# Kernel optimization log

Hardware: AMD Instinct MI355X
Metric: run time of the kernel (lower is better)

The kernel has to match this reference:

```python
import math
import jax, jax.numpy as jnp
import numpy as np

B, N, C = 2, 2048, 1024
H = 16
D = C // H  # 64
LN_EPS = 1e-5


def setup_inputs() -> dict:
    key = jax.random.key(0)
    ks = jax.random.split(key, 5)
    x = jax.random.normal(ks[0], (B, N, C), dtype=jnp.float32)
    w_qkv = jax.random.normal(ks[1], (C, 3 * C), dtype=jnp.float32) * 0.02
    w_proj = jax.random.normal(ks[2], (C, C), dtype=jnp.float32) * 0.02
    b_proj = jnp.zeros((C,), dtype=jnp.float32)
    ln_w = jnp.ones((D,), dtype=jnp.float32) + jax.random.normal(ks[3], (D,), dtype=jnp.float32) * 0.02
    ln_b = jax.random.normal(ks[4], (D,), dtype=jnp.float32) * 0.02
    return {"x": x, "w_qkv": w_qkv, "w_proj": w_proj, "b_proj": b_proj,
            "ln_w": ln_w, "ln_b": ln_b}


def _layernorm(t, w, b):
    mu = jnp.mean(t, axis=-1, keepdims=True)
    var = jnp.var(t, axis=-1, keepdims=True)
    return (t - mu) * jax.lax.rsqrt(var + LN_EPS) * w + b


def reference(x, w_qkv, w_proj, b_proj, ln_w, ln_b):
    b, n, c = x.shape
    h, d = H, c // H
    # QKV projection (no bias): [b,n,3c] -> [3,b,h,n,d]
    qkv = (x @ w_qkv).reshape(b, n, 3, h, d).transpose(2, 0, 3, 1, 4)
    q, k, v = qkv[0], qkv[1], qkv[2]
    # per-head LayerNorm on q and k (qk_norm)
    q = _layernorm(q, ln_w, ln_b)
    k = _layernorm(k, ln_w, ln_b)
    # NOTE: source multiplies q by sqrt(head_dim) (faithful to original)
    q = q * jnp.asarray(math.sqrt(d), dtype=q.dtype)
    scores = jnp.einsum('bhnd,bhmd->bhnm', q, k)  # [b,h,n,n]
    mask_value = -jnp.finfo(scores.dtype).max
    causal = jnp.tril(jnp.ones((n, n), dtype=bool))
    scores = jnp.where(causal, scores, mask_value)
    attn = jax.nn.softmax(scores, axis=-1)
    out = jnp.einsum('bhnm,bhmd->bhnd', attn, v)  # [b,h,n,d]
    out = out.transpose(0, 2, 1, 3).reshape(b, n, c)  # b n (h d)
    return out @ w_proj + b_proj
```

## Files before the change

### kernel.cpp

```cpp
#include <hip/hip_runtime.h>

#define LOG2E 1.4426950408889634f

typedef _Float16 f16x8_t __attribute__((ext_vector_type(8)));
typedef _Float16 f16x4_t __attribute__((ext_vector_type(4)));
typedef float    f32x4_t __attribute__((ext_vector_type(4)));

#define MFMA32(a, b, c) __builtin_amdgcn_mfma_f32_16x16x32_f16(a, b, c, 0, 0, 0)
#define MFMA16(a, b, c) __builtin_amdgcn_mfma_f32_16x16x16f16(a, b, c, 0, 0, 0)

__device__ __forceinline__ void async_copy16(void* lds, const void* g) {
    __builtin_amdgcn_global_load_lds(
        (const __attribute__((address_space(1))) unsigned char*)g,
        (__attribute__((address_space(3))) unsigned char*)lds, 16, 0, 0);
}

__global__ void cast_f32_f16_k(const float* __restrict__ in, _Float16* __restrict__ out, int n4) {
    int i = blockIdx.x * blockDim.x + threadIdx.x;
    if (i >= n4) return;
    float4 v = ((const float4*)in)[i];
    f16x4_t o = { (_Float16)v.x, (_Float16)v.y, (_Float16)v.z, (_Float16)v.w };
    ((f16x4_t*)out)[i] = o;
}

__global__ void transpose_cast_k(const float* __restrict__ in, _Float16* __restrict__ out,
                                 int R, int C) {
    __shared__ _Float16 tl[64][65];
    const int t = threadIdx.x;
    const int c = t & 63;
    const int r4 = t >> 6;
    const int r0 = blockIdx.y * 64, c0 = blockIdx.x * 64;
#pragma unroll
    for (int i = 0; i < 16; ++i) {
        int r = r4 + i * 4;
        tl[c][r] = (_Float16)in[(size_t)(r0 + r) * C + c0 + c];
    }
    __syncthreads();
#pragma unroll
    for (int i = 0; i < 16; ++i) {
        int rr = r4 + i * 4;
        out[(size_t)(c0 + rr) * R + r0 + c] = tl[rr][c];
    }
}

__global__ void vtrans_k(const _Float16* __restrict__ qkv, _Float16* __restrict__ VTg) {
    __shared__ _Float16 tl[64][65];
    const int t = threadIdx.x;
    const int bh = blockIdx.x;
    const int b = bh >> 4, h = bh & 15;
    const int n0 = blockIdx.y * 64;
    const int c = t & 63;
    const int r4 = t >> 6;
#pragma unroll
    for (int i = 0; i < 16; ++i) {
        int r = r4 + i * 4;
        tl[c][r] = qkv[(size_t)(b * 2048 + n0 + r) * 3072 + 2048 + h * 64 + c];
    }
    __syncthreads();
#pragma unroll
    for (int i = 0; i < 16; ++i) {
        int d = r4 + i * 4;
        VTg[(size_t)bh * 131072 + (size_t)d * 2048 + n0 + c] = tl[d][c];
    }
}

template <typename OutT, bool BIAS>
__global__ __launch_bounds__(256, 2)
void gemm_f16_k(const _Float16* __restrict__ A, const _Float16* __restrict__ BT,
                OutT* __restrict__ C, const float* __restrict__ bias,
                int M, int N, int K) {
    __shared__ _Float16 As[2][128][32];
    __shared__ _Float16 Bs[2][128][32];
    const int tid = threadIdx.x;
    const int wid = tid >> 6, lane = tid & 63;
    const int qd = lane >> 4, ln = lane & 15;
    const int m0 = blockIdx.x * 128, n0 = blockIdx.y * 128;
    const int wm = (wid >> 1) * 64, wn = (wid & 1) * 64;

    f32x4_t acc[4][4] = {};

    const int srow = lane >> 2;
    const int skk  = (lane & 3) * 8;

    for (int k0 = 0; k0 < K; k0 += 64) {
        __syncthreads();
#pragma unroll
        for (int p = 0; p < 4; ++p) {
            const int seg = p * 4 + wid;
            const int s   = seg >> 3;
            const int rg  = seg & 7;
            const int row = rg * 16 + srow;
            const size_t goff = (size_t)row * K + k0 + s * 32 + skk;
            async_copy16(&As[0][0][0] + seg * 512, A  + (size_t)m0 * K + goff);
            async_copy16(&Bs[0][0][0] + seg * 512, BT + (size_t)n0 * K + goff);
        }
        __syncthreads();
#pragma unroll
        for (int s = 0; s < 2; ++s) {
            f16x8_t a[4], b[4];
#pragma unroll
            for (int i = 0; i < 4; ++i)
                a[i] = *(const f16x8_t*)&As[s][wm + i * 16 + ln][qd * 8];
#pragma unroll
            for (int j = 0; j < 4; ++j)
                b[j] = *(const f16x8_t*)&Bs[s][wn + j * 16 + ln][qd * 8];
#pragma unroll
            for (int i = 0; i < 4; ++i)
#pragma unroll
                for (int j = 0; j < 4; ++j)
                    acc[i][j] = MFMA32(a[i], b[j], acc[i][j]);
        }
    }
#pragma unroll
    for (int i = 0; i < 4; ++i)
#pragma unroll
        for (int j = 0; j < 4; ++j) {
            const int col = n0 + wn + j * 16 + ln;
            const float bv = BIAS ? bias[col] : 0.0f;
#pragma unroll
            for (int r = 0; r < 4; ++r) {
                const int row = m0 + wm + i * 16 + qd * 4 + r;
                C[(size_t)row * N + col] = (OutT)(acc[i][j][r] + bv);
            }
        }
}

__global__ __launch_bounds__(256, 2)
void gemm_f16_m64_k(const _Float16* __restrict__ A, const _Float16* __restrict__ BT,
                    float* __restrict__ C, const float* __restrict__ bias,
                    int M, int N, int K) {
    __shared__ _Float16 As[2][64][32];
    __shared__ _Float16 Bs[2][128][32];
    const int tid = threadIdx.x;
    const int wid = tid >> 6, lane = tid & 63;
    const int qd = lane >> 4, ln = lane & 15;
    const int m0 = blockIdx.x * 64, n0 = blockIdx.y * 128;
    const int wn = wid * 32;

    f32x4_t acc[4][2] = {};
    const int srow = lane >> 2;
    const int skk  = (lane & 3) * 8;

    for (int k0 = 0; k0 < K; k0 += 64) {
        __syncthreads();
#pragma unroll
        for (int p = 0; p < 2; ++p) {
            const int seg = p * 4 + wid;
            const int hidx = seg * 512 + lane * 8;
            const int s_ = hidx >> 11;
            const int row = (hidx >> 5) & 63;
            const int kk = hidx & 31;
            async_copy16(&As[0][0][0] + seg * 512,
                         A + (size_t)(m0 + row) * K + k0 + s_ * 32 + kk);
        }
#pragma unroll
        for (int p = 0; p < 4; ++p) {
            const int seg = p * 4 + wid;
            const int s   = seg >> 3;
            const int rg  = seg & 7;
            const int row = rg * 16 + srow;
            async_copy16(&Bs[0][0][0] + seg * 512,
                         BT + (size_t)(n0 + row) * K + k0 + s * 32 + skk);
        }
        __syncthreads();
#pragma unroll
        for (int s = 0; s < 2; ++s) {
            f16x8_t a[4], b[2];
#pragma unroll
            for (int i = 0; i < 4; ++i)
                a[i] = *(const f16x8_t*)&As[s][i * 16 + ln][qd * 8];
#pragma unroll
            for (int j = 0; j < 2; ++j)
                b[j] = *(const f16x8_t*)&Bs[s][wn + j * 16 + ln][qd * 8];
#pragma unroll
            for (int i = 0; i < 4; ++i)
#pragma unroll
                for (int j = 0; j < 2; ++j)
                    acc[i][j] = MFMA32(a[i], b[j], acc[i][j]);
        }
    }
#pragma unroll
    for (int i = 0; i < 4; ++i)
#pragma unroll
        for (int j = 0; j < 2; ++j) {
            const int col = n0 + wn + j * 16 + ln;
            const float bv = bias[col];
#pragma unroll
            for (int r = 0; r < 4; ++r) {
                const int row = m0 + i * 16 + qd * 4 + r;
                C[(size_t)row * N + col] = acc[i][j][r] + bv;
            }
        }
}

__global__ void ln_qk_k(const _Float16* __restrict__ qkv, const float* __restrict__ ln_w,
                        const float* __restrict__ ln_b, _Float16* __restrict__ Qb,
                        _Float16* __restrict__ Kb) {
    const int tid = threadIdx.x;
    const int wid = tid >> 6, lane = tid & 63;
    const int row = blockIdx.x * 4 + wid;
    const int t = row >> 4;
    const int h = row & 15;
    const int b = t >> 11, n = t & 2047;
    const size_t base = (size_t)t * 3072 + h * 64 + lane;
    float q = (float)qkv[base];
    float k = (float)qkv[base + 1024];
    const float wv = ln_w[lane], bv = ln_b[lane];

    float sq = q, sk = k;
#pragma unroll
    for (int m = 1; m < 64; m <<= 1) { sq += __shfl_xor(sq, m); sk += __shfl_xor(sk, m); }
    sq *= (1.0f / 64.0f); sk *= (1.0f / 64.0f);
    const float dq = q - sq, dk = k - sk;
    float vq = dq * dq, vk = dk * dk;
#pragma unroll
    for (int m = 1; m < 64; m <<= 1) { vq += __shfl_xor(vq, m); vk += __shfl_xor(vk, m); }
    vq *= (1.0f / 64.0f); vk *= (1.0f / 64.0f);
    const float yq = dq * rsqrtf(vq + 1e-5f) * wv + bv;
    const float yk = dk * rsqrtf(vk + 1e-5f) * wv + bv;
    const size_t obase = ((size_t)((b * 16 + h) * 2048 + n)) * 64 + lane;
    Qb[obase] = (_Float16)(yq * (8.0f * LOG2E));
    Kb[obase] = (_Float16)yk;
}

__global__ __launch_bounds__(256, 3)
void attn_part_k(const _Float16* __restrict__ Q, const _Float16* __restrict__ K,
                 const _Float16* __restrict__ VTg, _Float16* __restrict__ O,
                 float* __restrict__ Op, float* __restrict__ ml) {
    __shared__ _Float16 Ks[2][2][64][32];
    __shared__ _Float16 VT[2][64][64];

    const int tid = threadIdx.x;
    const int wid = tid >> 6, lane = tid & 63;
    const int qd = lane >> 4, ln = lane & 15;
    const int bh = blockIdx.x;
    const int b = bh >> 4, h = bh & 15;
    const int y = blockIdx.y;
    int band, chunk, nst;
    if (y < 16)      { band = 16 + y; chunk = 0; nst = 16; }
    else if (y < 32) { band = 47 - y; chunk = 1; nst = band - 15; }
    else             { band = 47 - y; chunk = 0; nst = band + 1; }
    const size_t kvbase = (size_t)bh * 2048 * 64;
    const size_t vtbase = (size_t)bh * 131072;
    const int qrow0 = band * 64 + wid * 16;
    const int kvbeg = chunk * 1024;

    f16x8_t qf[2];
#pragma unroll
    for (int s = 0; s < 2; ++s)
        qf[s] = *(const f16x8_t*)&Q[kvbase + (size_t)(qrow0 + ln) * 64 + s * 32 + qd * 8];

    f32x4_t o[4] = {};
    float m = -3.0e38f, l = 0.0f;

    const int vrow = lane >> 3;
    const int vY   = (lane & 7) ^ (vrow & 7);
    const int khidx_base = lane * 8;

    auto stage = [&](int buf, int kv0) {
#pragma unroll
        for (int p = 0; p < 2; ++p) {
            const int seg = p * 4 + wid;
            const int hidx = seg * 512 + khidx_base;
            const int s_ = hidx >> 11;
            const int rrow = (hidx >> 5) & 63;
            const int kk = hidx & 31;
            async_copy16(&Ks[buf][0][0][0] + seg * 512,
                         K + kvbase + (size_t)(kv0 + rrow) * 64 + s_ * 32 + kk);
        }
#pragma unroll
        for (int p = 0; p < 2; ++p) {
            const int seg = p * 4 + wid;
            const int d = seg * 8 + vrow;
            async_copy16(&VT[buf][0][0] + seg * 512,
                         VTg + vtbase + (size_t)d * 2048 + kv0 + vY * 8);
        }
    };

    stage(0, kvbeg);

    for (int st = 0; st < nst; ++st) {
        const int kv0 = kvbeg + st * 64;
        __syncthreads();
        if (st + 1 < nst) stage((st + 1) & 1, kv0 + 64);
        const int buf = st & 1;

        f16x8_t kb[4][2];
#pragma unroll
        for (int jt = 0; jt < 4; ++jt)
#pragma unroll
            for (int s = 0; s < 2; ++s)
                kb[jt][s] = *(const f16x8_t*)&Ks[buf][s][jt * 16 + ln][qd * 8];
        f16x4_t vf[4][4];
#pragma unroll
        for (int dt = 0; dt < 4; ++dt)
#pragma unroll
            for (int c = 0; c < 4; ++c)
                vf[dt][c] = *(const f16x4_t*)
                    &VT[buf][dt * 16 + ln][(((2 * c + (qd >> 1)) ^ (ln & 7)) << 3) + (qd & 1) * 4];

        f32x4_t sc[4];
#pragma unroll
        for (int jt = 0; jt < 4; ++jt) {
            f32x4_t s = {};
            s = MFMA32(kb[jt][0], qf[0], s);
            s = MFMA32(kb[jt][1], qf[1], s);
            sc[jt] = s;
        }
        if (chunk * 16 + st == band) {
            const int qq = qrow0 + ln;
#pragma unroll
            for (int c = 0; c < 4; ++c)
#pragma unroll
                for (int r = 0; r < 4; ++r)
                    if (kv0 + c * 16 + qd * 4 + r > qq) sc[c][r] = -3.0e38f;
        }
        float mx = sc[0][0];
#pragma unroll
        for (int c = 0; c < 4; ++c)
#pragma unroll
            for (int r = 0; r < 4; ++r) mx = fmaxf(mx, sc[c][r]);
        mx = fmaxf(mx, __shfl_xor(mx, 16));
        mx = fmaxf(mx, __shfl_xor(mx, 32));
        const float mn = fmaxf(m, mx);
        const float al = exp2f(m - mn);
        m = mn;
        float rs = 0.0f;
        f16x4_t pf[4];
#pragma unroll
        for (int c = 0; c < 4; ++c)
#pragma unroll
            for (int r = 0; r < 4; ++r) {
                const float p = exp2f(sc[c][r] - mn);
                rs += p;
                pf[c][r] = (_Float16)p;
            }
        l = l * al + rs;
#pragma unroll
        for (int dt = 0; dt < 4; ++dt) o[dt] *= al;
#pragma unroll
        for (int dt = 0; dt < 4; ++dt)
#pragma unroll
            for (int c = 0; c < 4; ++c)
                o[dt] = MFMA16(vf[dt][c], pf[c], o[dt]);
    }

    float lt = l + __shfl_xor(l, 16);
    lt = lt + __shfl_xor(lt, 32);

    if (band < 16) {
        const float inv = 1.0f / lt;
        const size_t base = ((size_t)(b * 2048 + qrow0 + ln)) * 1024 + h * 64 + qd * 4;
#pragma unroll
        for (int dt = 0; dt < 4; ++dt) {
            f16x4_t ov;
#pragma unroll
            for (int r = 0; r < 4; ++r) ov[r] = (_Float16)(o[dt][r] * inv);
            *(f16x4_t*)&O[base + dt * 16] = ov;
        }
    } else {
        const size_t pb = (((size_t)bh * 16 + (band - 16)) * 2 + chunk);
        const int row = wid * 16 + ln;
        float* op = Op + pb * 4096 + (size_t)row * 64 + qd * 4;
#pragma unroll
        for (int dt = 0; dt < 4; ++dt)
            *(f32x4_t*)&op[dt * 16] = o[dt];
        if (qd == 0) {
            ml[pb * 128 + row * 2]     = m;
            ml[pb * 128 + row * 2 + 1] = lt;
        }
    }
}

__global__ __launch_bounds__(256)
void attn_merge_k(const float* __restrict__ Op, const float* __restrict__ ml,
                  _Float16* __restrict__ O) {
    const int bh = blockIdx.x, bnd = blockIdx.y;
    const int b = bh >> 4, h = bh & 15;
    const int band = 16 + bnd;
    const size_t pb = ((size_t)bh * 16 + bnd) * 2;
    const int tid = threadIdx.x;
    const int row = tid >> 2;
    const int c4 = (tid & 3) * 16;
    const float m0 = ml[pb * 128 + row * 2],     l0 = ml[pb * 128 + row * 2 + 1];
    const float m1 = ml[pb * 128 + 128 + row * 2], l1 = ml[pb * 128 + 128 + row * 2 + 1];
    const float mm = fmaxf(m0, m1);
    const float a0 = exp2f(m0 - mm), a1 = exp2f(m1 - mm);
    const float inv = 1.0f / (l0 * a0 + l1 * a1);
    const float* p0 = Op + pb * 4096 + (size_t)row * 64 + c4;
    const float* p1 = p0 + 4096;
    _Float16* op = O + ((size_t)(b * 2048 + band * 64 + row)) * 1024 + h * 64 + c4;
#pragma unroll
    for (int g = 0; g < 4; ++g) {
        f32x4_t v0 = *(const f32x4_t*)&p0[g * 4];
        f32x4_t v1 = *(const f32x4_t*)&p1[g * 4];
        f16x4_t ov;
#pragma unroll
        for (int r = 0; r < 4; ++r)
            ov[r] = (_Float16)((v0[r] * a0 + v1[r] * a1) * inv);
        *(f16x4_t*)&op[g * 4] = ov;
    }
}

extern "C" void kernel_launch(void* const* d_in, const int* in_sizes, int n_in,
                              void* d_out, int out_size, void* d_ws, size_t ws_size,
                              hipStream_t stream) {
    const float* x      = (const float*)d_in[0];
    const float* w_qkv  = (const float*)d_in[1];
    const float* w_proj = (const float*)d_in[2];
    const float* b_proj = (const float*)d_in[3];
    const float* ln_w   = (const float*)d_in[4];
    const float* ln_b   = (const float*)d_in[5];
    float* out = (float*)d_out;

    char* w = (char*)d_ws;
    _Float16*  qkv    = (_Float16*)w;  w += (size_t)4096 * 3072 * 2;
    _Float16*  xh     = (_Float16*)w;  w += (size_t)4096 * 1024 * 2;
    _Float16*  wqkvT  = (_Float16*)w;  w += (size_t)3072 * 1024 * 2;
    _Float16*  wprojT = (_Float16*)w;  w += (size_t)1024 * 1024 * 2;
    _Float16*  Qb     = (_Float16*)w;  w += (size_t)32 * 2048 * 64 * 2;
    _Float16*  Kb     = (_Float16*)w;  w += (size_t)32 * 2048 * 64 * 2;
    _Float16*  VTg    = (_Float16*)w;  w += (size_t)32 * 64 * 2048 * 2;
    _Float16*  Ah     = (_Float16*)w;  w += (size_t)4096 * 1024 * 2;
    float*     Op     = (float*)w;     w += (size_t)32 * 16 * 2 * 4096 * 4;
    float*     mlb    = (float*)w;     w += (size_t)32 * 16 * 2 * 128 * 4;

    cast_f32_f16_k<<<4096, 256, 0, stream>>>(x, xh, 4096 * 1024 / 4);
    transpose_cast_k<<<dim3(48, 16), 256, 0, stream>>>(w_qkv, wqkvT, 1024, 3072);
    transpose_cast_k<<<dim3(16, 16), 256, 0, stream>>>(w_proj, wprojT, 1024, 1024);
    gemm_f16_k<_Float16, false><<<dim3(32, 24), 256, 0, stream>>>(xh, wqkvT, qkv, nullptr, 4096, 3072, 1024);
    vtrans_k<<<dim3(32, 32), 256, 0, stream>>>(qkv, VTg);
    ln_qk_k<<<16384, 256, 0, stream>>>(qkv, ln_w, ln_b, Qb, Kb);
    attn_part_k<<<dim3(32, 48), 256, 0, stream>>>(Qb, Kb, VTg, Ah, Op, mlb);
    attn_merge_k<<<dim3(32, 16), 256, 0, stream>>>(Op, mlb, Ah);
    gemm_f16_m64_k<<<dim3(64, 8), 256, 0, stream>>>(Ah, wprojT, out, b_proj, 4096, 1024, 1024);
}
```

Before: 210.0 us.

## Widen attention query tile to 128 rows and pre-swizzle V tiles in global

The attention kernel now has each wave handle 32 query rows (two 16-row fragments), so every staged K/V tile is reused across twice as many queries. The causal work split is rebalanced into 128-row bands, with long bands split across two KV chunks and later merged. vtrans_k now writes V^T in tile-contiguous, pre-swizzled order, so staging becomes a linear copy and LDS reads use 8-wide vectors. Softmax probabilities are packed with cvt_pkrtz. In exchange, register pressure grows and the grid has fewer blocks, which may lower occupancy and worsen load balance.

```diff
diff --git a/kernel.cpp b/kernel.cpp
--- a/kernel.cpp
+++ b/kernel.cpp
@@ -4,6 +4,7 @@
 
 typedef _Float16 f16x8_t __attribute__((ext_vector_type(8)));
 typedef _Float16 f16x4_t __attribute__((ext_vector_type(4)));
+typedef _Float16 f16x2_t __attribute__((ext_vector_type(2)));
 typedef float    f32x4_t __attribute__((ext_vector_type(4)));
 
 #define MFMA32(a, b, c) __builtin_amdgcn_mfma_f32_16x16x32_f16(a, b, c, 0, 0, 0)
@@ -44,23 +45,30 @@
 }
 
 __global__ void vtrans_k(const _Float16* __restrict__ qkv, _Float16* __restrict__ VTg) {
-    __shared__ _Float16 tl[64][65];
-    const int t = threadIdx.x;
+    __shared__ _Float16 tl[64][68];
+    const int tid = threadIdx.x;
     const int bh = blockIdx.x;
     const int b = bh >> 4, h = bh & 15;
-    const int n0 = blockIdx.y * 64;
-    const int c = t & 63;
-    const int r4 = t >> 6;
+    const int t = blockIdx.y;
+    const int c = tid & 63;
+    const int r4 = tid >> 6;
 #pragma unroll
     for (int i = 0; i < 16; ++i) {
         int r = r4 + i * 4;
-        tl[c][r] = qkv[(size_t)(b * 2048 + n0 + r) * 3072 + 2048 + h * 64 + c];
+        tl[c][r] = qkv[(size_t)(b * 2048 + t * 64 + r) * 3072 + 2048 + h * 64 + c];
     }
     __syncthreads();
-#pragma unroll
-    for (int i = 0; i < 16; ++i) {
-        int d = r4 + i * 4;
-        VTg[(size_t)bh * 131072 + (size_t)d * 2048 + n0 + c] = tl[d][c];
+    const size_t obase = (size_t)bh * 131072 + (size_t)t * 4096;
+#pragma unroll
+    for (int e = 0; e < 2; ++e) {
+        const int ci = tid * 2 + e;
+        const int d = ci >> 3, w = ci & 7;
+        const int pq = w ^ (d & 7);
+        const int base = (pq >> 2) * 32 + (pq & 3) * 4;
+        f16x4_t v0 = *(const f16x4_t*)&tl[d][base];
+        f16x4_t v1 = *(const f16x4_t*)&tl[d][base + 16];
+        f16x8_t val = __builtin_shufflevector(v0, v1, 0, 1, 2, 3, 4, 5, 6, 7);
+        *(f16x8_t*)&VTg[obase + ci * 8] = val;
     }
 }
 
@@ -236,32 +244,28 @@
     const int bh = blockIdx.x;
     const int b = bh >> 4, h = bh & 15;
     const int y = blockIdx.y;
-    int band, chunk, nst;
-    if (y < 16)      { band = 16 + y; chunk = 0; nst = 16; }
-    else if (y < 32) { band = 47 - y; chunk = 1; nst = band - 15; }
-    else             { band = 47 - y; chunk = 0; nst = band + 1; }
+    int band, chunk, nst, kvbeg;
+    if (y < 16) { band = 15 - (y >> 1); chunk = y & 1; nst = band + 1; kvbeg = chunk * nst * 64; }
+    else        { band = 7 - (y - 16);  chunk = -1;    nst = 2 * (band + 1); kvbeg = 0; }
     const size_t kvbase = (size_t)bh * 2048 * 64;
     const size_t vtbase = (size_t)bh * 131072;
-    const int qrow0 = band * 64 + wid * 16;
-    const int kvbeg = chunk * 1024;
-
-    f16x8_t qf[2];
-#pragma unroll
-    for (int s = 0; s < 2; ++s)
-        qf[s] = *(const f16x8_t*)&Q[kvbase + (size_t)(qrow0 + ln) * 64 + s * 32 + qd * 8];
-
-    f32x4_t o[4] = {};
-    float m = -3.0e38f, l = 0.0f;
-
-    const int vrow = lane >> 3;
-    const int vY   = (lane & 7) ^ (vrow & 7);
-    const int khidx_base = lane * 8;
+    const int qrow0 = band * 128 + wid * 32;
+
+    f16x8_t qf[2][2];
+#pragma unroll
+    for (int f = 0; f < 2; ++f)
+#pragma unroll
+        for (int s = 0; s < 2; ++s)
+            qf[f][s] = *(const f16x8_t*)&Q[kvbase + (size_t)(qrow0 + f * 16 + ln) * 64 + s * 32 + qd * 8];
+
+    f32x4_t o[2][4] = {};
+    float m[2] = { -3.0e38f, -3.0e38f }, l[2] = { 0.0f, 0.0f };
 
     auto stage = [&](int buf, int kv0) {
 #pragma unroll
         for (int p = 0; p < 2; ++p) {
-            const int seg = p * 4 + wid;
-            const int hidx = seg * 512 + khidx_base;
+            const int seg = wid * 2 + p;
+            const int hidx = seg * 512 + lane * 8;
             const int s_ = hidx >> 11;
             const int rrow = (hidx >> 5) & 63;
             const int kk = hidx & 31;
@@ -270,10 +274,9 @@
         }
 #pragma unroll
         for (int p = 0; p < 2; ++p) {
-            const int seg = p * 4 + wid;
-            const int d = seg * 8 + vrow;
+            const int seg = wid * 2 + p;
             async_copy16(&VT[buf][0][0] + seg * 512,
-                         VTg + vtbase + (size_t)d * 2048 + kv0 + vY * 8);
+                         VTg + vtbase + (size_t)kv0 * 64 + seg * 512 + lane * 8);
         }
     };
 
@@ -291,83 +294,97 @@
 #pragma unroll
             for (int s = 0; s < 2; ++s)
                 kb[jt][s] = *(const f16x8_t*)&Ks[buf][s][jt * 16 + ln][qd * 8];
-        f16x4_t vf[4][4];
+        f16x8_t vf8[4][2];
 #pragma unroll
         for (int dt = 0; dt < 4; ++dt)
 #pragma unroll
+            for (int pp = 0; pp < 2; ++pp) {
+                const int w = (pp * 4 + qd) ^ (ln & 7);
+                vf8[dt][pp] = *(const f16x8_t*)&VT[buf][dt * 16 + ln][w * 8];
+            }
+
+#pragma unroll
+        for (int f = 0; f < 2; ++f) {
+            f32x4_t sc[4];
+#pragma unroll
+            for (int jt = 0; jt < 4; ++jt) {
+                f32x4_t s = {};
+                s = MFMA32(kb[jt][0], qf[f][0], s);
+                s = MFMA32(kb[jt][1], qf[f][1], s);
+                sc[jt] = s;
+            }
+            const int qbase = qrow0 + f * 16;
+            if (kv0 + 63 > qbase) {
+                const int qq = qbase + ln;
+#pragma unroll
+                for (int c = 0; c < 4; ++c)
+#pragma unroll
+                    for (int r = 0; r < 4; ++r)
+                        if (kv0 + c * 16 + qd * 4 + r > qq) sc[c][r] = -3.0e38f;
+            }
+            float mx = sc[0][0];
+#pragma unroll
             for (int c = 0; c < 4; ++c)
-                vf[dt][c] = *(const f16x4_t*)
-                    &VT[buf][dt * 16 + ln][(((2 * c + (qd >> 1)) ^ (ln & 7)) << 3) + (qd & 1) * 4];
-
-        f32x4_t sc[4];
-#pragma unroll
-        for (int jt = 0; jt < 4; ++jt) {
-            f32x4_t s = {};
-            s = MFMA32(kb[jt][0], qf[0], s);
-            s = MFMA32(kb[jt][1], qf[1], s);
-            sc[jt] = s;
-        }
-        if (chunk * 16 + st == band) {
-            const int qq = qrow0 + ln;
-#pragma unroll
-            for (int c = 0; c < 4; ++c)
-#pragma unroll
-                for (int r = 0; r < 4; ++r)
-                    if (kv0 + c * 16 + qd * 4 + r > qq) sc[c][r] = -3.0e38f;
-        }
-        float mx = sc[0][0];
-#pragma unroll
-        for (int c = 0; c < 4; ++c)
-#pragma unroll
-            for (int r = 0; r < 4; ++r) mx = fmaxf(mx, sc[c][r]);
-        mx = fmaxf(mx, __shfl_xor(mx, 16));
-        mx = fmaxf(mx, __shfl_xor(mx, 32));
-        const float mn = fmaxf(m, mx);
-        const float al = exp2f(m - mn);
-        m = mn;
-        float rs = 0.0f;
-        f16x4_t pf[4];
-#pragma unroll
-        for (int c = 0; c < 4; ++c)
-#pragma unroll
-            for (int r = 0; r < 4; ++r) {
-                const float p = exp2f(sc[c][r] - mn);
-                rs += p;
-                pf[c][r] = (_Float16)p;
-            }
-        l = l * al + rs;
-#pragma unroll
-        for (int dt = 0; dt < 4; ++dt) o[dt] *= al;
-#pragma unroll
-        for (int dt = 0; dt < 4; ++dt)
-#pragma unroll
-            for (int c = 0; c < 4; ++c)
-                o[dt] = MFMA16(vf[dt][c], pf[c], o[dt]);
-    }
-
-    float lt = l + __shfl_xor(l, 16);
-    lt = lt + __shfl_xor(lt, 32);
-
-    if (band < 16) {
-        const float inv = 1.0f / lt;
-        const size_t base = ((size_t)(b * 2048 + qrow0 + ln)) * 1024 + h * 64 + qd * 4;
-#pragma unroll
-        for (int dt = 0; dt < 4; ++dt) {
-            f16x4_t ov;
-#pragma unroll
-            for (int r = 0; r < 4; ++r) ov[r] = (_Float16)(o[dt][r] * inv);
-            *(f16x4_t*)&O[base + dt * 16] = ov;
-        }
-    } else {
-        const size_t pb = (((size_t)bh * 16 + (band - 16)) * 2 + chunk);
-        const int row = wid * 16 + ln;
-        float* op = Op + pb * 4096 + (size_t)row * 64 + qd * 4;
-#pragma unroll
-        for (int dt = 0; dt < 4; ++dt)
-            *(f32x4_t*)&op[dt * 16] = o[dt];
-        if (qd == 0) {
-            ml[pb * 128 + row * 2]     = m;
-            ml[pb * 128 + row * 2 + 1] = lt;
+#pragma unroll
+                for (int r = 0; r < 4; ++r) mx = fmaxf(mx, sc[c][r]);
+            mx = fmaxf(mx, __shfl_xor(mx, 16));
+            mx = fmaxf(mx, __shfl_xor(mx, 32));
+            const float mn = fmaxf(m[f], mx);
+            const float al = exp2f(m[f] - mn);
+            m[f] = mn;
+            float rs = 0.0f;
+            f16x4_t pf[4];
+#pragma unroll
+            for (int c = 0; c < 4; ++c) {
+                float p0 = exp2f(sc[c][0] - mn);
+                float p1 = exp2f(sc[c][1] - mn);
+                float p2 = exp2f(sc[c][2] - mn);
+                float p3 = exp2f(sc[c][3] - mn);
+                rs += (p0 + p1) + (p2 + p3);
+                f16x2_t a = __builtin_bit_cast(f16x2_t, __builtin_amdgcn_cvt_pkrtz(p0, p1));
+                f16x2_t bb = __builtin_bit_cast(f16x2_t, __builtin_amdgcn_cvt_pkrtz(p2, p3));
+                pf[c] = __builtin_shufflevector(a, bb, 0, 1, 2, 3);
+            }
+            l[f] = l[f] * al + rs;
+#pragma unroll
+            for (int dt = 0; dt < 4; ++dt) o[f][dt] *= al;
+#pragma unroll
+            for (int dt = 0; dt < 4; ++dt)
+#pragma unroll
+                for (int pp = 0; pp < 2; ++pp) {
+                    f16x4_t lo = __builtin_shufflevector(vf8[dt][pp], vf8[dt][pp], 0, 1, 2, 3);
+                    f16x4_t hi = __builtin_shufflevector(vf8[dt][pp], vf8[dt][pp], 4, 5, 6, 7);
+                    o[f][dt] = MFMA16(lo, pf[pp * 2 + 0], o[f][dt]);
+                    o[f][dt] = MFMA16(hi, pf[pp * 2 + 1], o[f][dt]);
+                }
+        }
+    }
+
+#pragma unroll
+    for (int f = 0; f < 2; ++f) {
+        float lt = l[f] + __shfl_xor(l[f], 16);
+        lt = lt + __shfl_xor(lt, 32);
+        if (chunk < 0) {
+            const float inv = 1.0f / lt;
+            const size_t base = ((size_t)(b * 2048 + qrow0 + f * 16 + ln)) * 1024 + h * 64 + qd * 4;
+#pragma unroll
+            for (int dt = 0; dt < 4; ++dt) {
+                f16x4_t ov;
+#pragma unroll
+                for (int r = 0; r < 4; ++r) ov[r] = (_Float16)(o[f][dt][r] * inv);
+                *(f16x4_t*)&O[base + dt * 16] = ov;
+            }
+        } else {
+            const size_t u = ((size_t)bh * 8 + (band - 8)) * 2 + chunk;
+            const int rowi = wid * 32 + f * 16 + ln;
+            float* op = Op + u * 8192 + (size_t)rowi * 64 + qd * 4;
+#pragma unroll
+            for (int dt = 0; dt < 4; ++dt)
+                *(f32x4_t*)&op[dt * 16] = o[f][dt];
+            if (qd == 0) {
+                ml[u * 256 + rowi * 2]     = m[f];
+                ml[u * 256 + rowi * 2 + 1] = lt;
+            }
         }
     }
 }
@@ -375,23 +392,23 @@
 __global__ __launch_bounds__(256)
 void attn_merge_k(const float* __restrict__ Op, const float* __restrict__ ml,
                   _Float16* __restrict__ O) {
-    const int bh = blockIdx.x, bnd = blockIdx.y;
+    const int bh = blockIdx.x, sb = blockIdx.y;
     const int b = bh >> 4, h = bh & 15;
-    const int band = 16 + bnd;
-    const size_t pb = ((size_t)bh * 16 + bnd) * 2;
-    const int tid = threadIdx.x;
-    const int row = tid >> 2;
-    const int c4 = (tid & 3) * 16;
-    const float m0 = ml[pb * 128 + row * 2],     l0 = ml[pb * 128 + row * 2 + 1];
-    const float m1 = ml[pb * 128 + 128 + row * 2], l1 = ml[pb * 128 + 128 + row * 2 + 1];
+    const int band = 8 + sb;
+    const size_t u = ((size_t)bh * 8 + sb) * 2;
+    const int tid = threadIdx.x;
+    const int row = tid >> 1;
+    const int d0 = (tid & 1) * 32;
+    const float m0 = ml[u * 256 + row * 2],       l0 = ml[u * 256 + row * 2 + 1];
+    const float m1 = ml[(u + 1) * 256 + row * 2], l1 = ml[(u + 1) * 256 + row * 2 + 1];
     const float mm = fmaxf(m0, m1);
     const float a0 = exp2f(m0 - mm), a1 = exp2f(m1 - mm);
     const float inv = 1.0f / (l0 * a0 + l1 * a1);
-    const float* p0 = Op + pb * 4096 + (size_t)row * 64 + c4;
-    const float* p1 = p0 + 4096;
-    _Float16* op = O + ((size_t)(b * 2048 + band * 64 + row)) * 1024 + h * 64 + c4;
-#pragma unroll
-    for (int g = 0; g < 4; ++g) {
+    const float* p0 = Op + u * 8192 + (size_t)row * 64 + d0;
+    const float* p1 = p0 + 8192;
+    _Float16* op = O + ((size_t)(b * 2048 + band * 128 + row)) * 1024 + h * 64 + d0;
+#pragma unroll
+    for (int g = 0; g < 8; ++g) {
         f32x4_t v0 = *(const f32x4_t*)&p0[g * 4];
         f32x4_t v1 = *(const f32x4_t*)&p1[g * 4];
         f16x4_t ov;
@@ -422,8 +439,8 @@
     _Float16*  Kb     = (_Float16*)w;  w += (size_t)32 * 2048 * 64 * 2;
     _Float16*  VTg    = (_Float16*)w;  w += (size_t)32 * 64 * 2048 * 2;
     _Float16*  Ah     = (_Float16*)w;  w += (size_t)4096 * 1024 * 2;
-    float*     Op     = (float*)w;     w += (size_t)32 * 16 * 2 * 4096 * 4;
-    float*     mlb    = (float*)w;     w += (size_t)32 * 16 * 2 * 128 * 4;
+    float*     Op     = (float*)w;     w += (size_t)32 * 8 * 2 * 8192 * 4;
+    float*     mlb    = (float*)w;     w += (size_t)32 * 8 * 2 * 256 * 4;
 
     cast_f32_f16_k<<<4096, 256, 0, stream>>>(x, xh, 4096 * 1024 / 4);
     transpose_cast_k<<<dim3(48, 16), 256, 0, stream>>>(w_qkv, wqkvT, 1024, 3072);
@@ -431,7 +448,7 @@
     gemm_f16_k<_Float16, false><<<dim3(32, 24), 256, 0, stream>>>(xh, wqkvT, qkv, nullptr, 4096, 3072, 1024);
     vtrans_k<<<dim3(32, 32), 256, 0, stream>>>(qkv, VTg);
     ln_qk_k<<<16384, 256, 0, stream>>>(qkv, ln_w, ln_b, Qb, Kb);
-    attn_part_k<<<dim3(32, 48), 256, 0, stream>>>(Qb, Kb, VTg, Ah, Op, mlb);
-    attn_merge_k<<<dim3(32, 16), 256, 0, stream>>>(Op, mlb, Ah);
+    attn_part_k<<<dim3(32, 24), 256, 0, stream>>>(Qb, Kb, VTg, Ah, Op, mlb);
+    attn_merge_k<<<dim3(32, 8), 256, 0, stream>>>(Op, mlb, Ah);
     gemm_f16_m64_k<<<dim3(64, 8), 256, 0, stream>>>(Ah, wprojT, out, b_proj, 4096, 1024, 1024);
 }
```

New measurement: 232.7 us. 1.11x slower.
